# Optimization experiments

Measured on AMD Instinct MI355X. Metric: run time of the kernel, lower is better.

Reference implementation:

```python
import jax, jax.numpy as jnp
import numpy as np

B, N, DIM, H, HD, COND, BS = 2, 1024, 768, 12, 64, 128, 16
S = 2 * N  # noised tokens [0:N) concatenated with clean x0 tokens [N:2N)
EPS = 1e-5
NEG = -1e30


def setup_inputs() -> dict:
    key = jax.random.key(0)
    ks = jax.random.split(key, 8)
    d = {}
    d['x'] = jax.random.normal(ks[0], (B, S, DIM), jnp.float32)
    d['c'] = jax.random.normal(ks[1], (B, COND), jnp.float32)
    # Rotary table for positions 0..N-1 (each half of the 2N sequence reuses the same positions)
    inv_freq = 1.0 / (10000.0 ** (np.arange(0, HD, 2, dtype=np.float64) / HD))
    freqs = np.arange(N, dtype=np.float64)[:, None] * inv_freq[None, :]
    emb = np.concatenate([freqs, freqs], axis=-1)  # [N, HD]
    cos = np.tile(np.cos(emb), (2, 1))[None, :, None, None, :]
    sin = np.tile(np.sin(emb), (2, 1))[None, :, None, None, :]
    d['cos'] = jnp.asarray(cos, jnp.float32)
    d['sin'] = jnp.asarray(sin, jnp.float32)
    # block-causal diffusion mask (flex_attention_mask): same (block, x0-flag) OR
    # cross-attention from noised block q>0 to strictly earlier CLEAN (x0) blocks
    idx = np.arange(S)
    fl = (idx >= N).astype(np.int64)
    blk = np.where(fl == 1, (idx - N) // BS, idx // BS)
    same = (blk[:, None] == blk[None, :]) & (fl[:, None] == fl[None, :])
    allowed = (blk[:, None] > 0) & (blk[None, :] < blk[:, None]) & (fl[None, :] == 1)
    d['mask'] = jnp.asarray(same | allowed)
    # parameters (adaLN is zero-init in the source; randomized here so the block is non-trivial)
    w = 0.02
    d['norm1_w'] = jnp.ones((DIM,), jnp.float32)
    d['qkv_w'] = jax.random.normal(ks[2], (3 * DIM, DIM), jnp.float32) * w
    d['attn_out_w'] = jax.random.normal(ks[3], (DIM, DIM), jnp.float32) * w
    d['norm2_w'] = jnp.ones((DIM,), jnp.float32)
    d['mlp_w1'] = jax.random.normal(ks[4], (4 * DIM, DIM), jnp.float32) * w
    d['mlp_b1'] = jnp.zeros((4 * DIM,), jnp.float32)
    d['mlp_w2'] = jax.random.normal(ks[5], (DIM, 4 * DIM), jnp.float32) * w
    d['mlp_b2'] = jnp.zeros((DIM,), jnp.float32)
    d['adaLN_w'] = jax.random.normal(ks[6], (6 * DIM, COND), jnp.float32) * w
    d['adaLN_b'] = jax.random.normal(ks[7], (6 * DIM,), jnp.float32) * w
    return d


def _ln(x, w):
    # F.layer_norm (no bias) followed by learned scale, as in the custom LayerNorm
    mu = x.mean(-1, keepdims=True)
    xc = x - mu
    var = (xc * xc).mean(-1, keepdims=True)
    return xc * jax.lax.rsqrt(var + EPS) * w


def reference(x, c, cos, sin, mask, norm1_w, qkv_w, attn_out_w, norm2_w,
              mlp_w1, mlp_b1, mlp_w2, mlp_b2, adaLN_w, adaLN_b):
    # adaLN modulation: [B, 6*DIM] -> six [B, 1, DIM] chunks
    mods = c @ adaLN_w.T + adaLN_b
    (shift_msa, scale_msa, gate_msa,
     shift_mlp, scale_mlp, gate_mlp) = jnp.split(mods[:, None, :], 6, axis=-1)
    x_skip = x
    h = _ln(x, norm1_w) * (1.0 + scale_msa) + shift_msa  # modulate_fused
    # qkv projection + rotary (torchscript path: qkv*cos + rotate_half(qkv)*sin)
    qkv = (h @ qkv_w.T).reshape(x.shape[0], S, 3, H, HD)
    rot = jnp.concatenate([-qkv[..., HD // 2:], qkv[..., :HD // 2]], axis=-1)
    qkv = qkv * cos + rot * sin
    q, k, v = qkv[:, :, 0], qkv[:, :, 1], qkv[:, :, 2]
    # SDPA with the block-causal diffusion mask, scale 1/sqrt(head_dim)
    scores = jnp.einsum('bqhd,bkhd->bhqk', q, k) / np.sqrt(HD).astype(np.float32)
    scores = jnp.where(mask[None, None], scores, NEG)
    p = jax.nn.softmax(scores, axis=-1)
    a = jnp.einsum('bhqk,bkhd->bqhd', p, v).reshape(x.shape[0], S, DIM)
    # bias_dropout_add_scale (inference => no dropout): gate * attn_out + residual
    x = gate_msa * (a @ attn_out_w.T) + x_skip
    h2 = _ln(x, norm2_w) * (1.0 + scale_mlp) + shift_mlp
    m = jax.nn.gelu(h2 @ mlp_w1.T + mlp_b1, approximate=True) @ mlp_w2.T + mlp_b2
    return x + gate_mlp * m
```

## Files before the change

### kernel.cpp

```cpp
#include <hip/hip_runtime.h>
#include <hip/hip_bf16.h>

#define EPS 1e-5f

typedef __attribute__((ext_vector_type(8))) short bf16x8;
typedef __attribute__((ext_vector_type(4))) short bf16x4;
typedef __attribute__((ext_vector_type(4))) float f32x4;

__device__ __forceinline__ f32x4 mfma_bf16(bf16x8 a, bf16x8 b, f32x4 c) {
    return __builtin_amdgcn_mfma_f32_16x16x32_bf16(a, b, c, 0, 0, 0);
}

__device__ __forceinline__ void async_ld16(const void* g, void* l) {
    __builtin_amdgcn_global_load_lds(
        (const __attribute__((address_space(1))) void*)g,
        (__attribute__((address_space(3))) void*)l, 16, 0, 0);
}

__device__ __forceinline__ float fast_gelu(float v) {
    float z2 = 1.5957691216057308f * (v + 0.044715f * v * v * v);
    float e = __expf(z2);
    return v * e / (e + 1.f);
}

__device__ __forceinline__ float bf2f(short s) {
    union { float f; unsigned u; } v;
    v.u = ((unsigned)(unsigned short)s) << 16;
    return v.f;
}

__global__ void k_pre(const float* __restrict__ a, __hip_bfloat16* __restrict__ oa, int na,
                      const float* __restrict__ b, __hip_bfloat16* __restrict__ ob, int nb,
                      const float* __restrict__ c, __hip_bfloat16* __restrict__ oc, int nc,
                      const float* __restrict__ d, __hip_bfloat16* __restrict__ od, int nd,
                      const float* __restrict__ cond, const float* __restrict__ alw,
                      const float* __restrict__ alb, float* __restrict__ mods) {
    if (blockIdx.x >= 27648) {
        int i = (blockIdx.x - 27648) * 256 + threadIdx.x;
        int bb = i / 4608, row = i - bb * 4608;
        const float4* cv = (const float4*)(cond + bb * 128);
        const float4* wv = (const float4*)(alw + (long)row * 128);
        float acc = 0.f;
#pragma unroll
        for (int k = 0; k < 32; ++k) {
            float4 x = cv[k], y = wv[k];
            acc += x.x * y.x + x.y * y.y + x.z * y.z + x.w * y.w;
        }
        mods[i] = acc + alb[row];
        return;
    }
    int i = blockIdx.x * 256 + threadIdx.x;
    if (i < na) { oa[i] = __float2bfloat16(a[i]); return; }
    i -= na;
    if (i < nb) { ob[i] = __float2bfloat16(b[i]); return; }
    i -= nb;
    if (i < nc) { oc[i] = __float2bfloat16(c[i]); return; }
    i -= nc;
    if (i < nd) od[i] = __float2bfloat16(d[i]);
}

__global__ void k_ln_mod(const float* __restrict__ x, const float* __restrict__ w,
                         const float* __restrict__ mods, int shiftOff, int scaleOff,
                         __hip_bfloat16* __restrict__ out) {
    int token = blockIdx.x;
    int lane = threadIdx.x;
    const float4* xr = (const float4*)(x + (long)token * 768);
    float4 v0 = xr[lane], v1 = xr[lane + 64], v2 = xr[lane + 128];
    float s  = v0.x + v0.y + v0.z + v0.w + v1.x + v1.y + v1.z + v1.w + v2.x + v2.y + v2.z + v2.w;
    float ss = v0.x*v0.x + v0.y*v0.y + v0.z*v0.z + v0.w*v0.w
             + v1.x*v1.x + v1.y*v1.y + v1.z*v1.z + v1.w*v1.w
             + v2.x*v2.x + v2.y*v2.y + v2.z*v2.z + v2.w*v2.w;
#pragma unroll
    for (int m = 32; m >= 1; m >>= 1) { s += __shfl_xor(s, m); ss += __shfl_xor(ss, m); }
    float mu = s * (1.f / 768.f);
    float var = ss * (1.f / 768.f) - mu * mu;
    float rs = rsqrtf(var + EPS);
    int b = token >> 11;
    const float* sh = mods + b * 4608 + shiftOff;
    const float* sc = mods + b * 4608 + scaleOff;
    __hip_bfloat16* o = out + (long)token * 768;
    float4 vv[3] = {v0, v1, v2};
#pragma unroll
    for (int kk = 0; kk < 3; ++kk) {
        int cbase = (lane + 64 * kk) * 4;
        const float* p = (const float*)&vv[kk];
#pragma unroll
        for (int j = 0; j < 4; ++j) {
            int col = cbase + j;
            float hv = (p[j] - mu) * rs * w[col] * (1.f + sc[col]) + sh[col];
            o[col] = __float2bfloat16(hv);
        }
    }
}

__global__ void k_red(const __hip_bfloat16* __restrict__ p, const float* __restrict__ x2,
                      const float* __restrict__ mods, const float* __restrict__ bias,
                      float* __restrict__ out) {
    long base = ((long)blockIdx.x * 256 + threadIdx.x) * 4;
    int col = (int)(base % 768);
    int row = (int)(base / 768);
    int b = row >> 11;
    short4 a0 = *(const short4*)(p + base);
    short4 a1 = *(const short4*)(p + 3145728 + base);
    float4 xr = *(const float4*)(x2 + base);
    float4 gt = *(const float4*)(mods + b * 4608 + 3840 + col);
    float4 bs = *(const float4*)(bias + col);
    float4 o;
    o.x = xr.x + gt.x * (bf2f(a0.x) + bf2f(a1.x) + bs.x);
    o.y = xr.y + gt.y * (bf2f(a0.y) + bf2f(a1.y) + bs.y);
    o.z = xr.z + gt.z * (bf2f(a0.z) + bf2f(a1.z) + bs.z);
    o.w = xr.w + gt.w * (bf2f(a0.w) + bf2f(a1.w) + bs.w);
    *(float4*)(out + base) = o;
}

__global__ __launch_bounds__(256) void k_attn(
    const __hip_bfloat16* __restrict__ q, const __hip_bfloat16* __restrict__ k,
    const __hip_bfloat16* __restrict__ vT, __hip_bfloat16* __restrict__ out) {
    __shared__ __hip_bfloat16 KL[2][64 * 64];
    __shared__ __hip_bfloat16 VL[2][64 * 64];
    __shared__ __hip_bfloat16 P[4][16 * 68];
    int tid = threadIdx.x;
    int w = tid >> 6, lane = tid & 63, l15 = lane & 15, quad = lane >> 4;
    int idx = blockIdx.x;
    int bh = idx % 24;
    int gi = idx / 24;
    int b0 = 62 - 2 * gi;
    int fl = w & 1, blk = b0 + (w >> 1);
    int qblk = fl * 64 + blk;

    const __hip_bfloat16* Q = q + ((long)bh * 2048 + qblk * 16) * 64;
    bf16x8 qa = *(const bf16x8*)(Q + l15 * 64 + quad * 8);
    bf16x8 qb = *(const bf16x8*)(Q + l15 * 64 + 32 + quad * 8);
    const __hip_bfloat16* K = k + (long)bh * 2048 * 64;
    const __hip_bfloat16* V = vT + (long)bh * 64 * 2048;

    auto kbase = [&](int t) -> int {
        if (t < b0 + 2) return 1024 + t * 16;
        if (t == b0 + 2) return b0 * 16;
        if (t == b0 + 3) return (b0 + 1) * 16;
        return 0;
    };
    auto active = [&](int t) -> bool {
        if (w == 0) return t < b0 || t == b0 + 2;
        if (w == 1) return t < b0 + 1;
        if (w == 2) return t < b0 + 1 || t == b0 + 3;
        return t < b0 + 2;
    };

    int kkr[2], kbs[2], vsi[2], vki[2];
#pragma unroll
    for (int i = 0; i < 2; ++i) {
        int o = i * 4096 + tid * 16;
        kkr[i] = o >> 7;
        int b = o & 127;
        kbs[i] = b ^ ((kkr[i] & 7) << 4);
        int lk2 = b ^ ((kkr[i] & 7) << 4);
        vsi[i] = lk2 >> 5;
        vki[i] = (lk2 & 31) >> 1;
    }
    auto stage = [&](int ci, int buf) {
#pragma unroll
        for (int i = 0; i < 2; ++i) {
            int gk = kbase(4 * ci + (kkr[i] >> 4)) + (kkr[i] & 15);
            async_ld16(K + (long)gk * 64 + (kbs[i] >> 1),
                       (char*)&KL[buf][0] + i * 4096 + tid * 16);
        }
#pragma unroll
        for (int i = 0; i < 2; ++i) {
            int gk = kbase(4 * ci + vsi[i]) + vki[i];
            async_ld16(V + (long)kkr[i] * 2048 + gk,
                       (char*)&VL[buf][0] + i * 4096 + tid * 16);
        }
    };

    int kfo[4][2], vfo[2][4];
#pragma unroll
    for (int s = 0; s < 4; ++s)
#pragma unroll
        for (int h = 0; h < 2; ++h)
            kfo[s][h] = (s * 16 + l15) * 64 +
                        (((h * 64 + quad * 16) ^ ((l15 & 7) << 4)) >> 1);
#pragma unroll
    for (int p2 = 0; p2 < 2; ++p2)
#pragma unroll
        for (int tt = 0; tt < 4; ++tt) {
            int d = tt * 16 + l15;
            int c = (p2 * 64 + (quad >> 1) * 32 + (quad & 1) * 16) ^ ((l15 & 7) << 4);
            vfo[p2][tt] = d * 64 + (c >> 1);
        }

    const f32x4 vzero = {0.f, 0.f, 0.f, 0.f};
    f32x4 o[4]; float l[4];
#pragma unroll
    for (int rr = 0; rr < 4; ++rr) { o[rr] = vzero; l[rr] = 0.f; }

    int nIter = (b0 + 7) >> 2;
    __hip_bfloat16* Pw = &P[w][0];

    bf16x8 paP[2];
    bf16x8 vfP[2][4];

    stage(0, 0);
    for (int ci = 0; ci < nIter; ++ci) {
        int cb = ci & 1;
        if (ci > 0) asm volatile("s_barrier" ::: "memory");
        if (ci + 1 < nIter) {
            stage(ci + 1, cb ^ 1);
            asm volatile("s_waitcnt vmcnt(4)" ::: "memory");
        } else {
            asm volatile("s_waitcnt vmcnt(0)" ::: "memory");
        }
        asm volatile("s_barrier" ::: "memory");

        bf16x8 ka[4], kb8[4];
#pragma unroll
        for (int s = 0; s < 4; ++s) {
            ka[s]  = *(const bf16x8*)&KL[cb][kfo[s][0]];
            kb8[s] = *(const bf16x8*)&KL[cb][kfo[s][1]];
        }
        f32x4 sc[4];
        __builtin_amdgcn_s_setprio(1);
#pragma unroll
        for (int s = 0; s < 4; ++s)
            sc[s] = mfma_bf16(qb, kb8[s], mfma_bf16(qa, ka[s], vzero));
        __builtin_amdgcn_s_setprio(0);
        bf16x8 vf[2][4];
#pragma unroll
        for (int p2 = 0; p2 < 2; ++p2)
#pragma unroll
            for (int tt = 0; tt < 4; ++tt)
                vf[p2][tt] = *(const bf16x8*)&VL[cb][vfo[p2][tt]];

#pragma unroll
        for (int s = 0; s < 4; ++s) {
            bool a = active(4 * ci + s);
#pragma unroll
            for (int rr = 0; rr < 4; ++rr) {
                float pv = a ? __expf(sc[s][rr]) : 0.f;
                l[rr] += pv;
                Pw[(quad * 4 + rr) * 68 + s * 16 + l15] = __float2bfloat16(pv);
            }
        }
        if (ci > 0) {
            __builtin_amdgcn_s_setprio(1);
#pragma unroll
            for (int p2 = 0; p2 < 2; ++p2)
#pragma unroll
                for (int tt = 0; tt < 4; ++tt)
                    o[tt] = mfma_bf16(paP[p2], vfP[p2][tt], o[tt]);
            __builtin_amdgcn_s_setprio(0);
        }
        asm volatile("s_waitcnt lgkmcnt(0)" ::: "memory");
        bf16x8 pa[2];
#pragma unroll
        for (int p2 = 0; p2 < 2; ++p2) {
            union { bf16x4 h[2]; bf16x8 v; } u;
            u.h[0] = *(const bf16x4*)(Pw + l15 * 68 + p2 * 32 + quad * 8);
            u.h[1] = *(const bf16x4*)(Pw + l15 * 68 + p2 * 32 + quad * 8 + 4);
            pa[p2] = u.v;
        }
#pragma unroll
        for (int p2 = 0; p2 < 2; ++p2) {
            paP[p2] = pa[p2];
#pragma unroll
            for (int tt = 0; tt < 4; ++tt) vfP[p2][tt] = vf[p2][tt];
        }
    }
    asm volatile("s_waitcnt lgkmcnt(0)" ::: "memory");
    __builtin_amdgcn_s_setprio(1);
#pragma unroll
    for (int p2 = 0; p2 < 2; ++p2)
#pragma unroll
        for (int tt = 0; tt < 4; ++tt)
            o[tt] = mfma_bf16(paP[p2], vfP[p2][tt], o[tt]);
    __builtin_amdgcn_s_setprio(0);

    int b = bh / 12, h = bh - b * 12;
    int seqbase = qblk * 16;
#pragma unroll
    for (int rr = 0; rr < 4; ++rr) {
        float lr = l[rr];
#pragma unroll
        for (int msk = 1; msk < 16; msk <<= 1) lr += __shfl_xor(lr, msk, 16);
        float inv = 1.f / lr;
        long row = b * 2048 + seqbase + quad * 4 + rr;
#pragma unroll
        for (int tt = 0; tt < 4; ++tt)
            out[row * 768 + h * 64 + tt * 16 + l15] = __float2bfloat16(o[tt][rr] * inv);
    }
}

template <int MODE, int TN>
__global__ __launch_bounds__(TN == 128 ? 256 : 128) void k_gemm(
    const __hip_bfloat16* __restrict__ A, const __hip_bfloat16* __restrict__ W,
    float* __restrict__ Cf, __hip_bfloat16* __restrict__ Cb,
    const float* __restrict__ bias, const float* __restrict__ mods, int gateOff,
    const float* __restrict__ resid, const float* __restrict__ cosb,
    const float* __restrict__ sinb, __hip_bfloat16* __restrict__ qo,
    __hip_bfloat16* __restrict__ ko, __hip_bfloat16* __restrict__ vo,
    int M, int N, int K, int lda) {
    constexpr int NW = (TN == 128) ? 4 : 2;
    constexpr int ACH = 512 / (NW * 64);
    constexpr int BCH = (TN * 4) / (NW * 64);
    constexpr int NINST = ACH + BCH;
    __shared__ __hip_bfloat16 lA[2][128 * 32];
    __shared__ __hip_bfloat16 lB[2][TN * 32];
    int t = threadIdx.x;
    int wave = t >> 6, lane = t & 63, l15 = lane & 15, quad = lane >> 4;
    int wr = (TN == 128) ? (wave >> 1) : wave;
    int wc = (TN == 128) ? (wave & 1) : 0;
    int sw8 = (quad ^ ((l15 >> 1) & 3)) * 8;
    long bm = blockIdx.x, bn = blockIdx.y;
    const __hip_bfloat16* Ab = A + bm * 128 * lda + (long)blockIdx.z * K;
    const __hip_bfloat16* Wb = W + bn * TN * lda + (long)blockIdx.z * K;

    long soffA[ACH], soffB[BCH];
#pragma unroll
    for (int cc = 0; cc < ACH; ++cc) {
        int chunk = cc * NW * 64 + t;
        int row = chunk >> 2;
        int c = (chunk & 3) ^ ((row >> 1) & 3);
        soffA[cc] = (long)row * lda + c * 8;
    }
#pragma unroll
    for (int cc = 0; cc < BCH; ++cc) {
        int chunk = cc * NW * 64 + t;
        int row = chunk >> 2;
        int c = (chunk & 3) ^ ((row >> 1) & 3);
        soffB[cc] = (long)row * lda + c * 8;
    }
    auto stage = [&](int k0, int buf) {
        char* lAc = (char*)&lA[buf][0];
        char* lBc = (char*)&lB[buf][0];
#pragma unroll
        for (int cc = 0; cc < ACH; ++cc)
            async_ld16(Ab + soffA[cc] + k0, lAc + cc * (NW * 1024) + wave * 1024);
#pragma unroll
        for (int cc = 0; cc < BCH; ++cc)
            async_ld16(Wb + soffB[cc] + k0, lBc + cc * (NW * 1024) + wave * 1024);
    };

    f32x4 acc[4][4];
#pragma unroll
    for (int i = 0; i < 4; ++i)
#pragma unroll
        for (int j = 0; j < 4; ++j) acc[i][j] = (f32x4){0.f, 0.f, 0.f, 0.f};

    int nIter = K / 32;
    stage(0, 0);
    for (int i = 0; i < nIter; ++i) {
        int cb = i & 1;
        if (i > 0) asm volatile("s_barrier" ::: "memory");
        if (i + 1 < nIter) {
            stage((i + 1) * 32, cb ^ 1);
            asm volatile("s_waitcnt vmcnt(%0)" :: "n"(NINST) : "memory");
        } else {
            asm volatile("s_waitcnt vmcnt(0)" ::: "memory");
        }
        asm volatile("s_barrier" ::: "memory");
        bf16x8 af[4], bfr[4];
#pragma unroll
        for (int ii = 0; ii < 4; ++ii)
            af[ii] = *(const bf16x8*)&lA[cb][(wr * 64 + ii * 16 + l15) * 32 + sw8];
#pragma unroll
        for (int j = 0; j < 4; ++j)
            bfr[j] = *(const bf16x8*)&lB[cb][(wc * 64 + j * 16 + l15) * 32 + sw8];
#pragma unroll
        for (int ii = 0; ii < 4; ++ii)
#pragma unroll
            for (int j = 0; j < 4; ++j)
                acc[ii][j] = mfma_bf16(af[ii], bfr[j], acc[ii][j]);
    }

    if (MODE == 4) {
        int hcol = (int)bn * 2 + wc;
        int th = hcol / 12, h = hcol % 12;
#pragma unroll
        for (int i = 0; i < 4; ++i) {
#pragma unroll
            for (int r = 0; r < 4; ++r) {
                int row = (int)bm * 128 + wr * 64 + i * 16 + quad * 4 + r;
                int s = row & 2047, b = row >> 11;
                long bh_ = b * 12 + h;
                const float* cbp = cosb + s * 64;
                const float* sbp = sinb + s * 64;
#pragma unroll
                for (int j = 0; j < 2; ++j) {
                    int dh = j * 16 + l15;
                    float a0f = acc[i][j][r], a1f = acc[i][j + 2][r];
                    float o0 = a0f * cbp[dh] - a1f * sbp[dh];
                    float o1 = a1f * cbp[dh + 32] + a0f * sbp[dh + 32];
                    if (th == 0) {
                        __hip_bfloat16* d = qo + (bh_ * 2048 + s) * 64;
                        d[dh]      = __float2bfloat16(o0 * 0.125f);
                        d[dh + 32] = __float2bfloat16(o1 * 0.125f);
                    } else if (th == 1) {
                        __hip_bfloat16* d = ko + (bh_ * 2048 + s) * 64;
                        d[dh]      = __float2bfloat16(o0);
                        d[dh + 32] = __float2bfloat16(o1);
                    } else {
                        __hip_bfloat16* d = vo + bh_ * 64 * 2048 + s;
                        d[(long)dh * 2048]        = __float2bfloat16(o0);
                        d[(long)(dh + 32) * 2048] = __float2bfloat16(o1);
                    }
                }
            }
        }
        return;
    }

#pragma unroll
    for (int i = 0; i < 4; ++i) {
#pragma unroll
        for (int j = 0; j < 4; ++j) {
#pragma unroll
            for (int r = 0; r < 4; ++r) {
                int row = (int)bm * 128 + wr * 64 + i * 16 + quad * 4 + r;
                int col = (int)bn * TN + wc * 64 + j * 16 + l15;
                float v = acc[i][j][r];
                long idx = (long)row * N + col;
                if (MODE == 1) {
                    Cf[idx] = mods[(row >> 11) * 4608 + gateOff + col] * v + resid[idx];
                } else if (MODE == 2) {
                    Cb[idx] = __float2bfloat16(fast_gelu(v + bias[col]));
                } else if (MODE == 3) {
                    Cf[idx] = resid[idx] + mods[(row >> 11) * 4608 + gateOff + col] * (v + bias[col]);
                } else {
                    Cb[(long)blockIdx.z * M * N + idx] = __float2bfloat16(v);
                }
            }
        }
    }
}

extern "C" void kernel_launch(void* const* d_in, const int* in_sizes, int n_in,
                              void* d_out, int out_size, void* d_ws, size_t ws_size,
                              hipStream_t stream) {
    const float* x    = (const float*)d_in[0];
    const float* c    = (const float*)d_in[1];
    const float* cosb = (const float*)d_in[2];
    const float* sinb = (const float*)d_in[3];
    const float* n1w  = (const float*)d_in[5];
    const float* qkvw = (const float*)d_in[6];
    const float* aow  = (const float*)d_in[7];
    const float* n2w  = (const float*)d_in[8];
    const float* w1   = (const float*)d_in[9];
    const float* b1   = (const float*)d_in[10];
    const float* w2   = (const float*)d_in[11];
    const float* b2   = (const float*)d_in[12];
    const float* alw  = (const float*)d_in[13];
    const float* alb  = (const float*)d_in[14];

    char* ws = (char*)d_ws;
    size_t off = 0;
    auto alloc = [&](size_t bytes) -> void* {
        void* p = ws + off;
        off += (bytes + 255) & ~(size_t)255;
        return p;
    };
    float*          mods = (float*)alloc(2 * 4608 * 4);
    __hip_bfloat16* hbuf = (__hip_bfloat16*)alloc((size_t)4096 * 768 * 2);
    __hip_bfloat16* qb   = (__hip_bfloat16*)alloc((size_t)24 * 2048 * 64 * 2);
    __hip_bfloat16* kb   = (__hip_bfloat16*)alloc((size_t)24 * 2048 * 64 * 2);
    __hip_bfloat16* vT   = (__hip_bfloat16*)alloc((size_t)24 * 64 * 2048 * 2);
    __hip_bfloat16* abuf = (__hip_bfloat16*)alloc((size_t)4096 * 768 * 2);
    float*          x2   = (float*)alloc((size_t)4096 * 768 * 4);
    __hip_bfloat16* h2   = (__hip_bfloat16*)alloc((size_t)4096 * 768 * 2);
    __hip_bfloat16* m1   = (__hip_bfloat16*)alloc((size_t)4096 * 3072 * 2);
    __hip_bfloat16* m2p  = (__hip_bfloat16*)alloc((size_t)2 * 4096 * 768 * 2);
    __hip_bfloat16* wq   = (__hip_bfloat16*)alloc((size_t)2304 * 768 * 2);
    __hip_bfloat16* wa   = (__hip_bfloat16*)alloc((size_t)768 * 768 * 2);
    __hip_bfloat16* w1b  = (__hip_bfloat16*)alloc((size_t)3072 * 768 * 2);
    __hip_bfloat16* w2b  = (__hip_bfloat16*)alloc((size_t)768 * 3072 * 2);

    k_pre<<<27684, 256, 0, stream>>>(qkvw, wq, 2304 * 768, aow, wa, 768 * 768,
                                     w1, w1b, 3072 * 768, w2, w2b, 768 * 3072,
                                     c, alw, alb, mods);
    k_ln_mod<<<4096, 64, 0, stream>>>(x, n1w, mods, 0, 768, hbuf);
    k_gemm<4, 128><<<dim3(32, 18), 256, 0, stream>>>(hbuf, wq, nullptr, nullptr, nullptr, nullptr, 0,
                                                     nullptr, cosb, sinb, qb, kb, vT,
                                                     4096, 2304, 768, 768);
    k_attn<<<768, 256, 0, stream>>>(qb, kb, vT, abuf);
    k_gemm<1, 64><<<dim3(32, 12), 128, 0, stream>>>(abuf, wa, x2, nullptr, nullptr, mods, 1536,
                                                    x, nullptr, nullptr, nullptr, nullptr, nullptr,
                                                    4096, 768, 768, 768);
    k_ln_mod<<<4096, 64, 0, stream>>>(x2, n2w, mods, 2304, 3072, h2);
    k_gemm<2, 128><<<dim3(32, 24), 256, 0, stream>>>(h2, w1b, nullptr, m1, b1, nullptr, 0,
                                                     nullptr, nullptr, nullptr, nullptr, nullptr, nullptr,
                                                     4096, 3072, 768, 768);
    k_gemm<5, 128><<<dim3(32, 6, 2), 256, 0, stream>>>(m1, w2b, nullptr, m2p, nullptr, nullptr, 0,
                                                       nullptr, nullptr, nullptr, nullptr, nullptr, nullptr,
                                                       4096, 768, 1536, 3072);
    k_red<<<3072, 256, 0, stream>>>(m2p, x2, mods, b2, (float*)d_out);
}
```

Measured before the change: 292.6 us.

## Use 128x64 GEMM tiles everywhere and stage V-transpose stores through LDS

Every GEMM now uses the 128x64 tile with two waves, which doubles the grid size for the QKV, MLP1 and MLP2 launches. In the QKV epilogue each block now maps to exactly one head, so branching per element goes away. The V output is transposed through shared memory and written as coalesced 32-bit stores, replacing scattered strided bf16 stores. In exchange, each block reuses less data per loaded tile and reads more A-matrix traffic from global memory, but more blocks are available to keep the CUs busy.

```diff
diff --git a/kernel.cpp b/kernel.cpp
--- a/kernel.cpp
+++ b/kernel.cpp
@@ -27,6 +27,12 @@
     union { float f; unsigned u; } v;
     v.u = ((unsigned)(unsigned short)s) << 16;
     return v.f;
+}
+
+__device__ __forceinline__ short f2bf_s(float x) {
+    union { __hip_bfloat16 h; short s; } cv;
+    cv.h = __float2bfloat16(x);
+    return cv.s;
 }
 
 __global__ void k_pre(const float* __restrict__ a, __hip_bfloat16* __restrict__ oa, int na,
@@ -291,7 +297,7 @@
 }
 
 template <int MODE, int TN>
-__global__ __launch_bounds__(TN == 128 ? 256 : 128) void k_gemm(
+__global__ __launch_bounds__(128) void k_gemm(
     const __hip_bfloat16* __restrict__ A, const __hip_bfloat16* __restrict__ W,
     float* __restrict__ Cf, __hip_bfloat16* __restrict__ Cb,
     const float* __restrict__ bias, const float* __restrict__ mods, int gateOff,
@@ -299,16 +305,16 @@
     const float* __restrict__ sinb, __hip_bfloat16* __restrict__ qo,
     __hip_bfloat16* __restrict__ ko, __hip_bfloat16* __restrict__ vo,
     int M, int N, int K, int lda) {
-    constexpr int NW = (TN == 128) ? 4 : 2;
+    static_assert(TN == 64, "all GEMMs run the 64-tile now");
+    constexpr int NW = 2;
     constexpr int ACH = 512 / (NW * 64);
     constexpr int BCH = (TN * 4) / (NW * 64);
     constexpr int NINST = ACH + BCH;
-    __shared__ __hip_bfloat16 lA[2][128 * 32];
-    __shared__ __hip_bfloat16 lB[2][TN * 32];
+    constexpr int SM_SHORTS = 2 * 128 * 32 + 2 * TN * 32;
+    __shared__ __align__(16) __hip_bfloat16 SM[SM_SHORTS];
     int t = threadIdx.x;
     int wave = t >> 6, lane = t & 63, l15 = lane & 15, quad = lane >> 4;
-    int wr = (TN == 128) ? (wave >> 1) : wave;
-    int wc = (TN == 128) ? (wave & 1) : 0;
+    int wr = wave, wc = 0;
     int sw8 = (quad ^ ((l15 >> 1) & 3)) * 8;
     long bm = blockIdx.x, bn = blockIdx.y;
     const __hip_bfloat16* Ab = A + bm * 128 * lda + (long)blockIdx.z * K;
@@ -330,8 +336,8 @@
         soffB[cc] = (long)row * lda + c * 8;
     }
     auto stage = [&](int k0, int buf) {
-        char* lAc = (char*)&lA[buf][0];
-        char* lBc = (char*)&lB[buf][0];
+        char* lAc = (char*)(SM + buf * 4096);
+        char* lBc = (char*)(SM + 8192 + buf * (TN * 32));
 #pragma unroll
         for (int cc = 0; cc < ACH; ++cc)
             async_ld16(Ab + soffA[cc] + k0, lAc + cc * (NW * 1024) + wave * 1024);
@@ -361,10 +367,10 @@
         bf16x8 af[4], bfr[4];
 #pragma unroll
         for (int ii = 0; ii < 4; ++ii)
-            af[ii] = *(const bf16x8*)&lA[cb][(wr * 64 + ii * 16 + l15) * 32 + sw8];
+            af[ii] = *(const bf16x8*)&SM[cb * 4096 + (wr * 64 + ii * 16 + l15) * 32 + sw8];
 #pragma unroll
         for (int j = 0; j < 4; ++j)
-            bfr[j] = *(const bf16x8*)&lB[cb][(wc * 64 + j * 16 + l15) * 32 + sw8];
+            bfr[j] = *(const bf16x8*)&SM[8192 + cb * (TN * 32) + (j * 16 + l15) * 32 + sw8];
 #pragma unroll
         for (int ii = 0; ii < 4; ++ii)
 #pragma unroll
@@ -373,36 +379,60 @@
     }
 
     if (MODE == 4) {
-        int hcol = (int)bn * 2 + wc;
-        int th = hcol / 12, h = hcol % 12;
+        int th = (int)bn / 12, h = (int)bn % 12;
+        int sbase = ((int)bm * 128) & 2047;
+        int b = ((int)bm * 128) >> 11;
+        long bh_ = (long)b * 12 + h;
+        if (th == 2) {
+            __syncthreads();
+#pragma unroll
+            for (int i = 0; i < 4; ++i) {
+                int sl = wr * 64 + i * 16 + quad * 4;
+#pragma unroll
+                for (int j = 0; j < 2; ++j) {
+                    int dh = j * 16 + l15;
+                    bf16x4 p0, p1;
+#pragma unroll
+                    for (int r = 0; r < 4; ++r) {
+                        int s = sbase + sl + r;
+                        const float* cbp = cosb + s * 64;
+                        const float* sbp = sinb + s * 64;
+                        float a0f = acc[i][j][r], a1f = acc[i][j + 2][r];
+                        p0[r] = f2bf_s(a0f * cbp[dh] - a1f * sbp[dh]);
+                        p1[r] = f2bf_s(a1f * cbp[dh + 32] + a0f * sbp[dh + 32]);
+                    }
+                    *(bf16x4*)(SM + dh * 132 + sl) = p0;
+                    *(bf16x4*)(SM + (dh + 32) * 132 + sl) = p1;
+                }
+            }
+            __syncthreads();
+            __hip_bfloat16* dst = vo + bh_ * 64 * 2048;
+#pragma unroll
+            for (int dd = 0; dd < 32; ++dd) {
+                int d = wr * 32 + dd;
+                unsigned pv = *(const unsigned*)(SM + d * 132 + lane * 2);
+                *(unsigned*)(dst + (long)d * 2048 + sbase + lane * 2) = pv;
+            }
+            return;
+        }
+        float qs = (th == 0) ? 0.125f : 1.f;
+        __hip_bfloat16* base = (th == 0) ? qo : ko;
 #pragma unroll
         for (int i = 0; i < 4; ++i) {
 #pragma unroll
             for (int r = 0; r < 4; ++r) {
-                int row = (int)bm * 128 + wr * 64 + i * 16 + quad * 4 + r;
-                int s = row & 2047, b = row >> 11;
-                long bh_ = b * 12 + h;
+                int s = sbase + wr * 64 + i * 16 + quad * 4 + r;
                 const float* cbp = cosb + s * 64;
                 const float* sbp = sinb + s * 64;
+                __hip_bfloat16* d = base + (bh_ * 2048 + s) * 64;
 #pragma unroll
                 for (int j = 0; j < 2; ++j) {
                     int dh = j * 16 + l15;
                     float a0f = acc[i][j][r], a1f = acc[i][j + 2][r];
                     float o0 = a0f * cbp[dh] - a1f * sbp[dh];
                     float o1 = a1f * cbp[dh + 32] + a0f * sbp[dh + 32];
-                    if (th == 0) {
-                        __hip_bfloat16* d = qo + (bh_ * 2048 + s) * 64;
-                        d[dh]      = __float2bfloat16(o0 * 0.125f);
-                        d[dh + 32] = __float2bfloat16(o1 * 0.125f);
-                    } else if (th == 1) {
-                        __hip_bfloat16* d = ko + (bh_ * 2048 + s) * 64;
-                        d[dh]      = __float2bfloat16(o0);
-                        d[dh + 32] = __float2bfloat16(o1);
-                    } else {
-                        __hip_bfloat16* d = vo + bh_ * 64 * 2048 + s;
-                        d[(long)dh * 2048]        = __float2bfloat16(o0);
-                        d[(long)(dh + 32) * 2048] = __float2bfloat16(o1);
-                    }
+                    d[dh]      = __float2bfloat16(o0 * qs);
+                    d[dh + 32] = __float2bfloat16(o1 * qs);
                 }
             }
         }
@@ -416,15 +446,13 @@
 #pragma unroll
             for (int r = 0; r < 4; ++r) {
                 int row = (int)bm * 128 + wr * 64 + i * 16 + quad * 4 + r;
-                int col = (int)bn * TN + wc * 64 + j * 16 + l15;
+                int col = (int)bn * TN + j * 16 + l15;
                 float v = acc[i][j][r];
                 long idx = (long)row * N + col;
                 if (MODE == 1) {
                     Cf[idx] = mods[(row >> 11) * 4608 + gateOff + col] * v + resid[idx];
                 } else if (MODE == 2) {
                     Cb[idx] = __float2bfloat16(fast_gelu(v + bias[col]));
-                } else if (MODE == 3) {
-                    Cf[idx] = resid[idx] + mods[(row >> 11) * 4608 + gateOff + col] * (v + bias[col]);
                 } else {
                     Cb[(long)blockIdx.z * M * N + idx] = __float2bfloat16(v);
                 }
@@ -477,18 +505,18 @@
                                      w1, w1b, 3072 * 768, w2, w2b, 768 * 3072,
                                      c, alw, alb, mods);
     k_ln_mod<<<4096, 64, 0, stream>>>(x, n1w, mods, 0, 768, hbuf);
-    k_gemm<4, 128><<<dim3(32, 18), 256, 0, stream>>>(hbuf, wq, nullptr, nullptr, nullptr, nullptr, 0,
-                                                     nullptr, cosb, sinb, qb, kb, vT,
-                                                     4096, 2304, 768, 768);
+    k_gemm<4, 64><<<dim3(32, 36), 128, 0, stream>>>(hbuf, wq, nullptr, nullptr, nullptr, nullptr, 0,
+                                                    nullptr, cosb, sinb, qb, kb, vT,
+                                                    4096, 2304, 768, 768);
     k_attn<<<768, 256, 0, stream>>>(qb, kb, vT, abuf);
     k_gemm<1, 64><<<dim3(32, 12), 128, 0, stream>>>(abuf, wa, x2, nullptr, nullptr, mods, 1536,
                                                     x, nullptr, nullptr, nullptr, nullptr, nullptr,
                                                     4096, 768, 768, 768);
     k_ln_mod<<<4096, 64, 0, stream>>>(x2, n2w, mods, 2304, 3072, h2);
-    k_gemm<2, 128><<<dim3(32, 24), 256, 0, stream>>>(h2, w1b, nullptr, m1, b1, nullptr, 0,
-                                                     nullptr, nullptr, nullptr, nullptr, nullptr, nullptr,
-                                                     4096, 3072, 768, 768);
-    k_gemm<5, 128><<<dim3(32, 6, 2), 256, 0, stream>>>(m1, w2b, nullptr, m2p, nullptr, nullptr, 0,
+    k_gemm<2, 64><<<dim3(32, 48), 128, 0, stream>>>(h2, w1b, nullptr, m1, b1, nullptr, 0,
+                                                    nullptr, nullptr, nullptr, nullptr, nullptr, nullptr,
+                                                    4096, 3072, 768, 768);
+    k_gemm<5, 64><<<dim3(32, 12, 2), 128, 0, stream>>>(m1, w2b, nullptr, m2p, nullptr, nullptr, 0,
                                                        nullptr, nullptr, nullptr, nullptr, nullptr, nullptr,
                                                        4096, 768, 1536, 3072);
     k_red<<<3072, 256, 0, stream>>>(m2p, x2, mods, b2, (float*)d_out);
```

After: 288.5 us. No clear change (-1.4%).
